# Kernel tuning notes

Hardware: AMD Instinct MI355X
Metric: run time of the kernel (lower is better)

The kernel has to match this reference:

```python
import jax, jax.numpy as jnp
import numpy as np

N_ENT = 200000; N_REL = 500; D = 400; RAP = 16; RAD = 32; H = 4; ARITY = 4; B = 512; EPS = 1e-5


def _lin(x, w, b):
    return x @ w.T + b


def _ln(x, g, b):
    m = x.mean(-1, keepdims=True)
    v = x.var(-1, keepdims=True)
    return (x - m) / jnp.sqrt(v + EPS) * g + b


def _forward(ent_emb, rel_emb, pos_emb, relposw_w, relposw_b, relposinv_w, relposinv_b,
             relw4_w, relw4_b, q_w, q_b, k_w, k_b, v_w, v_b, fca_w, fca_b,
             ln1_g, ln1_b, ln2_g, ln2_b, w1_w, w1_b, w2_w, w2_b, fc_w, fc_b,
             posbn_g, posbn_b, bn_g, bn_b, bias, rel_idx, ent_idx):
    r0 = rel_emb[rel_idx]                                   # [B,D]
    e0 = ent_emb[ent_idx]                                   # [B,A-1,D]
    x0 = jnp.concatenate([r0[:, None, :], e0], axis=1) + pos_emb[:ARITY][None]
    # manual multi-head attention (separate q/k/v/fc linears)
    q = _lin(x0, q_w, q_b).reshape(B, ARITY, H, D)
    k = _lin(x0, k_w, k_b).reshape(B, ARITY, H, D)
    v = _lin(x0, v_w, v_b).reshape(B, ARITY, H, D)
    scale = jnp.float32(1.0 / np.sqrt(D))
    att = jax.nn.softmax(jnp.einsum('blhd,bmhd->bhlm', q, k) * scale, axis=-1)
    o = jnp.einsum('bhlm,bmhd->blhd', att, v).reshape(B, ARITY, H * D)
    x1 = _ln(x0 + _lin(o, fca_w, fca_b), ln1_g, ln1_b)
    # Conv1d kernel-size-1 FFN == pointwise linear
    ffn = _lin(jax.nn.relu(_lin(x1, w1_w, w1_b)), w2_w, w2_b)
    x2 = _ln(x1 + ffn, ln2_g, ln2_b)
    r = x2[:, 0, :]
    # RA_Position: relation-generated per-sample 1x1 grouped conv filters
    f = _lin(r, relposw_w, relposw_b)                       # [B,RAP]

    def ra_pos(e):
        # BatchNorm1d(num_features=1): batch stats over (batch, length)
        m = e.mean(); vv = e.var()
        xn = (e - m) / jnp.sqrt(vv + EPS) * posbn_g[0] + posbn_b[0]
        y = (f[:, :, None] * xn[:, None, :]).reshape(B, RAP * D)  # grouped conv1d k=1
        return _lin(y, relposinv_w, relposinv_b)            # [B,D]

    ef = jnp.stack([ra_pos(x2[:, i + 1, :]) for i in range(ARITY - 1)], axis=1)  # [B,3,D]
    # RADConv: torch .view(B,1,-1,arity-1) interleaves entities -> plain row-major reshape
    xr = ef.reshape(B, 1, D, ARITY - 1)
    m = xr.mean(); vv = xr.var()                            # BatchNorm2d(1), batch stats
    xn = (xr - m) / jnp.sqrt(vv + EPS) * bn_g[0] + bn_b[0]
    kern = _lin(r, relw4_w, relw4_b).reshape(B, RAD, ARITY - 1)
    conv = jnp.einsum('bkj,bij->bki', kern, xn[:, 0])       # grouped conv2d (1,A-1), valid
    pooled = conv.reshape(B, RAD, D // 2, 2).max(axis=-1).reshape(B, RAD * D // 2)
    h = jax.nn.relu(_lin(pooled, fc_w, fc_b))               # [B,D]
    return h @ ent_emb.T + bias                             # [B,N_ENT]


def setup_inputs() -> dict:
    key = jax.random.key(0)
    ks = iter(jax.random.split(key, 40))

    def nrm(shape, s=0.05):
        return jax.random.normal(next(ks), shape, jnp.float32) * s

    def lw(o, i):
        return jax.random.normal(next(ks), (o, i), jnp.float32) * (1.0 / np.sqrt(i)).astype(np.float32)

    return {
        'ent_emb': nrm((N_ENT, D)),
        'rel_emb': nrm((N_REL, D)),
        'pos_emb': nrm((9, D)),
        'relposw_w': lw(RAP, D), 'relposw_b': jnp.zeros((RAP,), jnp.float32),
        'relposinv_w': lw(D, RAP * D), 'relposinv_b': jnp.zeros((D,), jnp.float32),
        'relw4_w': lw(3 * RAD, D), 'relw4_b': jnp.zeros((3 * RAD,), jnp.float32),
        'q_w': lw(H * D, D), 'q_b': jnp.zeros((H * D,), jnp.float32),
        'k_w': lw(H * D, D), 'k_b': jnp.zeros((H * D,), jnp.float32),
        'v_w': lw(H * D, D), 'v_b': jnp.zeros((H * D,), jnp.float32),
        'fca_w': lw(D, H * D), 'fca_b': jnp.zeros((D,), jnp.float32),
        'ln1_g': jnp.ones((D,), jnp.float32), 'ln1_b': jnp.zeros((D,), jnp.float32),
        'ln2_g': jnp.ones((D,), jnp.float32), 'ln2_b': jnp.zeros((D,), jnp.float32),
        'w1_w': lw(2 * D, D), 'w1_b': jnp.zeros((2 * D,), jnp.float32),
        'w2_w': lw(D, 2 * D), 'w2_b': jnp.zeros((D,), jnp.float32),
        'fc_w': lw(D, RAD * D // 2), 'fc_b': jnp.zeros((D,), jnp.float32),
        'posbn_g': jnp.ones((1,), jnp.float32), 'posbn_b': jnp.zeros((1,), jnp.float32),
        'bn_g': jnp.ones((1,), jnp.float32), 'bn_b': jnp.zeros((1,), jnp.float32),
        'bias': jnp.zeros((N_ENT,), jnp.float32),
        'rel_idx': jax.random.randint(next(ks), (B,), 0, N_REL),
        'ent_idx': jax.random.randint(next(ks), (B, ARITY - 1), 0, N_ENT),
    }


def reference(ent_emb, rel_emb, pos_emb, relposw_w, relposw_b, relposinv_w, relposinv_b,
              relw4_w, relw4_b, q_w, q_b, k_w, k_b, v_w, v_b, fca_w, fca_b,
              ln1_g, ln1_b, ln2_g, ln2_b, w1_w, w1_b, w2_w, w2_b, fc_w, fc_b,
              posbn_g, posbn_b, bn_g, bn_b, bias, rel_idx, ent_idx):
    return _forward(ent_emb, rel_emb, pos_emb, relposw_w, relposw_b, relposinv_w, relposinv_b,
                    relw4_w, relw4_b, q_w, q_b, k_w, k_b, v_w, v_b, fca_w, fca_b,
                    ln1_g, ln1_b, ln2_g, ln2_b, w1_w, w1_b, w2_w, w2_b, fc_w, fc_b,
                    posbn_g, posbn_b, bn_g, bn_b, bias, rel_idx, ent_idx)
```

## Files before the change

### kernel.cpp

```cpp
#include <hip/hip_runtime.h>

typedef unsigned short u16;
typedef __attribute__((ext_vector_type(8))) short s8v;
typedef __attribute__((ext_vector_type(4))) float f4v;
typedef __attribute__((ext_vector_type(4))) unsigned int u32x4;

typedef const __attribute__((address_space(1))) unsigned gas_u32;
typedef __attribute__((address_space(3))) unsigned las_u32;

__device__ __forceinline__ float bf2f(u16 u) { return __uint_as_float(((unsigned)u) << 16); }
__device__ __forceinline__ u16 f2bf(float x) {
  unsigned b = __float_as_uint(x);
  return (u16)((b + 0x7FFFu + ((b >> 16) & 1u)) >> 16);
}

__global__ void convert_w_kernel(const float* __restrict__ src, u16* __restrict__ dst,
                                 int N, int Kreal, int KP) {
  int idx = blockIdx.x * 256 + threadIdx.x;
  if (idx >= N * KP) return;
  int n = idx / KP, k = idx % KP;
  dst[idx] = (k < Kreal) ? f2bf(src[(size_t)n * Kreal + k]) : (u16)0;
}

__global__ void build_x0_kernel(const float* __restrict__ ent_emb, const float* __restrict__ rel_emb,
                                const float* __restrict__ pos_emb, const int* __restrict__ rel_idx,
                                const int* __restrict__ ent_idx, u16* __restrict__ x0) {
  int idx = blockIdx.x * 256 + threadIdx.x;
  if (idx >= 512 * 4 * 400) return;
  int d = idx % 400;
  int l = (idx / 400) % 4;
  int b = idx / 1600;
  float v;
  if (l == 0) v = rel_emb[(size_t)rel_idx[b] * 400 + d];
  else        v = ent_emb[(size_t)ent_idx[b * 3 + l - 1] * 400 + d];
  x0[(size_t)(b * 4 + l) * 416 + d] = f2bf(v + pos_emb[l * 400 + d]);
}

template<bool BF32, bool RELU, bool OUTBF>
__global__ __launch_bounds__(256) void mfma_gemm(
    const u16* __restrict__ A, int lda,
    const void* __restrict__ Bp, int ldb,
    const float* __restrict__ bias,
    void* __restrict__ Cp, long long ldc,
    int N, int KP, int Kreal) {
  __shared__ u16 As[128 * 32];
  __shared__ u16 Bs[128 * 32];
  const int m0 = blockIdx.x * 128, n0 = blockIdx.y * 128;
  const int tid = threadIdx.x;
  const int lane = tid & 63, w = tid >> 6;
  const int mw = (w & 1) * 64, nw = (w >> 1) * 64;
  f4v acc[4][4] = {};

  const int arow = tid >> 2, akq = tid & 3;
  const u16* ag0 = A + (size_t)(m0 + arow) * lda + akq * 8;
  const u16* ag1 = A + (size_t)(m0 + 64 + arow) * lda + akq * 8;
  int br0 = n0 + arow;      if (br0 >= N) br0 = N - 1;
  int br1 = n0 + 64 + arow; if (br1 >= N) br1 = N - 1;
  const u16* bg0 = nullptr; const u16* bg1 = nullptr;
  if (!BF32) {
    bg0 = (const u16*)Bp + (size_t)br0 * ldb + akq * 8;
    bg1 = (const u16*)Bp + (size_t)br1 * ldb + akq * 8;
  }
  const float* Bf = (const float*)Bp;

  u16* lA0 = As + w * 512;
  u16* lA1 = As + 2048 + w * 512;
  u16* lB0 = Bs + w * 512;
  u16* lB1 = Bs + 2048 + w * 512;

  const u16* ap = As + (size_t)(mw + (lane & 15)) * 32 + (lane >> 4) * 8;
  const u16* bp = Bs + (size_t)(nw + (lane & 15)) * 32 + (lane >> 4) * 8;

  for (int k0 = 0; k0 < KP; k0 += 32) {
    __builtin_amdgcn_global_load_lds((gas_u32*)(ag0 + k0), (las_u32*)lA0, 16, 0, 0);
    __builtin_amdgcn_global_load_lds((gas_u32*)(ag1 + k0), (las_u32*)lA1, 16, 0, 0);
    if (BF32) {
      int kk = k0 + akq * 8;
#pragma unroll
      for (int t = 0; t < 2; ++t) {
        int rowg = t ? br1 : br0;
        const float* src = Bf + (size_t)rowg * ldb + kk;
        float4 v0 = (kk < Kreal)     ? *(const float4*)(src)     : make_float4(0.f, 0.f, 0.f, 0.f);
        float4 v1 = (kk + 4 < Kreal) ? *(const float4*)(src + 4) : make_float4(0.f, 0.f, 0.f, 0.f);
        u32x4 pk;
        pk.x = (unsigned)f2bf(v0.x) | ((unsigned)f2bf(v0.y) << 16);
        pk.y = (unsigned)f2bf(v0.z) | ((unsigned)f2bf(v0.w) << 16);
        pk.z = (unsigned)f2bf(v1.x) | ((unsigned)f2bf(v1.y) << 16);
        pk.w = (unsigned)f2bf(v1.z) | ((unsigned)f2bf(v1.w) << 16);
        *(u32x4*)(Bs + t * 2048 + tid * 8) = pk;
      }
    } else {
      __builtin_amdgcn_global_load_lds((gas_u32*)(bg0 + k0), (las_u32*)lB0, 16, 0, 0);
      __builtin_amdgcn_global_load_lds((gas_u32*)(bg1 + k0), (las_u32*)lB1, 16, 0, 0);
    }
    __syncthreads();
    s8v af[4], bf[4];
#pragma unroll
    for (int i = 0; i < 4; ++i) af[i] = *(const s8v*)(ap + i * 16 * 32);
#pragma unroll
    for (int j = 0; j < 4; ++j) bf[j] = *(const s8v*)(bp + j * 16 * 32);
#pragma unroll
    for (int i = 0; i < 4; ++i)
#pragma unroll
      for (int j = 0; j < 4; ++j)
        acc[i][j] = __builtin_amdgcn_mfma_f32_16x16x32_bf16(af[i], bf[j], acc[i][j], 0, 0, 0);
    __syncthreads();
  }

  const int quad = lane >> 4, col = lane & 15;
#pragma unroll
  for (int i = 0; i < 4; ++i) {
#pragma unroll
    for (int j = 0; j < 4; ++j) {
      int n = n0 + nw + 16 * j + col;
      if (n >= N) continue;
      float bv = bias[n];
#pragma unroll
      for (int r = 0; r < 4; ++r) {
        int m = m0 + mw + 16 * i + quad * 4 + r;
        float v = acc[i][j][r] + bv;
        if (RELU) v = fmaxf(v, 0.f);
        size_t off = (size_t)m * ldc + n;
        if (OUTBF) ((u16*)Cp)[off] = f2bf(v);
        else       ((float*)Cp)[off] = v;
      }
    }
  }
}

__global__ __launch_bounds__(256) void sgemm_valu(
    const u16* __restrict__ X, int lda,
    const float* __restrict__ W, const float* __restrict__ bvec,
    float* __restrict__ Y, int ldc, int M, int N, int K) {
  int n0 = blockIdx.x * 64, m0 = blockIdx.y * 64;
  __shared__ float Xs[16][64];
  __shared__ float Ws[16][64];
  int tid = threadIdx.x;
  int tx = tid & 15, ty = tid >> 4;
  int lr = tid >> 2, lc = (tid & 3) << 2;
  float acc[4][4] = {};
  const u16* xbase = X + (size_t)(m0 + lr) * lda + lc;
  int wn = n0 + lr;
  bool wvalid = wn < N;
  const float* wbase = W + (size_t)(wvalid ? wn : 0) * K + lc;
  for (int k0 = 0; k0 < K; k0 += 16) {
#pragma unroll
    for (int j = 0; j < 4; ++j) Xs[lc + j][lr] = bf2f(xbase[k0 + j]);
#pragma unroll
    for (int j = 0; j < 4; ++j) Ws[lc + j][lr] = wvalid ? wbase[k0 + j] : 0.f;
    __syncthreads();
#pragma unroll
    for (int kk = 0; kk < 16; ++kk) {
      float xv[4], wv[4];
#pragma unroll
      for (int a = 0; a < 4; ++a) xv[a] = Xs[kk][ty * 4 + a];
#pragma unroll
      for (int b = 0; b < 4; ++b) wv[b] = Ws[kk][tx * 4 + b];
#pragma unroll
      for (int a = 0; a < 4; ++a)
#pragma unroll
        for (int b = 0; b < 4; ++b)
          acc[a][b] = fmaf(xv[a], wv[b], acc[a][b]);
    }
    __syncthreads();
  }
#pragma unroll
  for (int a = 0; a < 4; ++a) {
    int m = m0 + ty * 4 + a;
#pragma unroll
    for (int b = 0; b < 4; ++b) {
      int n = n0 + tx * 4 + b;
      if (n < N) Y[(size_t)m * ldc + n] = acc[a][b] + bvec[n];
    }
  }
}

__device__ __forceinline__ float wave_sum(float v) {
#pragma unroll
  for (int o = 32; o > 0; o >>= 1) v += __shfl_xor(v, o);
  return v;
}

__global__ void score_kernel(const u16* __restrict__ qkv, float* __restrict__ att) {
  int bh = blockIdx.x;
  int h = bh & 3, b = bh >> 2;
  int lane = threadIdx.x;
  float s[4][4];
#pragma unroll
  for (int l = 0; l < 4; ++l) {
    const u16* qp = qkv + (size_t)(b * 4 + l) * 4800 + h * 400;
#pragma unroll
    for (int m = 0; m < 4; ++m) {
      const u16* kp = qkv + (size_t)(b * 4 + m) * 4800 + 1600 + h * 400;
      float p = 0.f;
      for (int d = lane; d < 400; d += 64) p += bf2f(qp[d]) * bf2f(kp[d]);
      s[l][m] = wave_sum(p) * 0.05f;
    }
  }
  if (lane < 16) {
    int l = lane >> 2, m = lane & 3;
    float mx = fmaxf(fmaxf(s[l][0], s[l][1]), fmaxf(s[l][2], s[l][3]));
    float e0 = expf(s[l][0] - mx), e1 = expf(s[l][1] - mx);
    float e2 = expf(s[l][2] - mx), e3 = expf(s[l][3] - mx);
    float inv = 1.f / (e0 + e1 + e2 + e3);
    float ev = (m == 0) ? e0 : (m == 1) ? e1 : (m == 2) ? e2 : e3;
    att[(size_t)bh * 16 + l * 4 + m] = ev * inv;
  }
}

__global__ void attn_apply_kernel(const float* __restrict__ att, const u16* __restrict__ qkv,
                                  u16* __restrict__ o) {
  int idx = blockIdx.x * 256 + threadIdx.x;
  if (idx >= 2048 * 1600) return;
  int col = idx % 1600;
  int row = idx / 1600;
  int b = row >> 2, l = row & 3, h = col / 400;
  const float* ap = att + ((size_t)b * 4 + h) * 16 + l * 4;
  float acc = 0.f;
#pragma unroll
  for (int m = 0; m < 4; ++m)
    acc += ap[m] * bf2f(qkv[(size_t)(b * 4 + m) * 4800 + 3200 + col]);
  o[idx] = f2bf(acc);
}

__global__ __launch_bounds__(128) void ln_kernel(const u16* __restrict__ A, int lda,
                                                 const float* __restrict__ Bv, int ldb,
                                                 const float* __restrict__ g, const float* __restrict__ beta,
                                                 u16* __restrict__ out, int ldo) {
  int row = blockIdx.x;
  int tid = threadIdx.x;
  const u16* a = A + (size_t)row * lda;
  const float* bb = Bv + (size_t)row * ldb;
  float vals[4] = {};
  float s = 0.f, q = 0.f;
#pragma unroll
  for (int j = 0; j < 4; ++j) {
    int d = tid + j * 128;
    if (d < 400) { float x = bf2f(a[d]) + bb[d]; vals[j] = x; s += x; q += x * x; }
  }
  __shared__ float rs[128], rq[128];
  rs[tid] = s; rq[tid] = q;
  __syncthreads();
  for (int off = 64; off > 0; off >>= 1) {
    if (tid < off) { rs[tid] += rs[tid + off]; rq[tid] += rq[tid + off]; }
    __syncthreads();
  }
  float mean = rs[0] * (1.f / 400.f);
  float var = rq[0] * (1.f / 400.f) - mean * mean;
  float rstd = rsqrtf(var + 1e-5f);
  u16* op = out + (size_t)row * ldo;
#pragma unroll
  for (int j = 0; j < 4; ++j) {
    int d = tid + j * 128;
    if (d < 400) op[d] = f2bf((vals[j] - mean) * rstd * g[d] + beta[d]);
  }
}

template<typename T>
__global__ __launch_bounds__(256) void stat_partial(const T* __restrict__ base, long long slice_stride,
                                                    int row_stride, int len, long long total, int nb,
                                                    float* __restrict__ sums) {
  int slice = blockIdx.x / nb, chunk = blockIdx.x % nb;
  const T* p = base + (size_t)slice * slice_stride;
  int tid = threadIdx.x;
  float s = 0.f, q = 0.f;
  long long step = (long long)nb * 256;
  for (long long t = (long long)chunk * 256 + tid; t < total; t += step) {
    int row = (int)(t / len), colx = (int)(t % len);
    float x;
    if (sizeof(T) == 2) x = bf2f(((const u16*)p)[(size_t)row * row_stride + colx]);
    else                x = ((const float*)p)[(size_t)row * row_stride + colx];
    s += x; q += x * x;
  }
  __shared__ float rs[256], rq[256];
  rs[tid] = s; rq[tid] = q;
  __syncthreads();
  for (int off = 128; off > 0; off >>= 1) {
    if (tid < off) { rs[tid] += rs[tid + off]; rq[tid] += rq[tid + off]; }
    __syncthreads();
  }
  if (tid == 0) {
    atomicAdd(&sums[2 * slice], rs[0]);
    atomicAdd(&sums[2 * slice + 1], rq[0]);
  }
}

__device__ __forceinline__ void mean_rstd(const float* sums, float count, float& m, float& rstd) {
  m = sums[0] / count;
  float var = sums[1] / count - m * m;
  rstd = rsqrtf(var + 1e-5f);
}

__global__ void build_y3_kernel(const u16* __restrict__ x2, const float* __restrict__ f,
                                const float* __restrict__ scal, const float* __restrict__ pg,
                                const float* __restrict__ pb, u16* __restrict__ y3) {
  int idx = blockIdx.x * 256 + threadIdx.x;
  if (idx >= 3 * 512 * 6400) return;
  int d = idx % 400;
  int p = (idx / 400) % 16;
  int b = (idx / 6400) % 512;
  int i = idx / (512 * 6400);
  float m, rstd;
  mean_rstd(scal + 2 * i, 204800.f, m, rstd);
  float e = bf2f(x2[(size_t)(b * 4 + i + 1) * 400 + d]);
  float xn = (e - m) * rstd * pg[0] + pb[0];
  y3[idx] = f2bf(f[b * 16 + p] * xn);
}

__global__ void convpool_kernel(const float* __restrict__ kern, const float* __restrict__ efI,
                                const float* __restrict__ scal, const float* __restrict__ bg_,
                                const float* __restrict__ bb_, u16* __restrict__ pooled) {
  int idx = blockIdx.x * 256 + threadIdx.x;
  if (idx >= 512 * 32 * 200) return;
  int i2 = idx % 200;
  int k = (idx / 200) % 32;
  int b = idx / 6400;
  float m, rstd;
  mean_rstd(scal, 614400.f, m, rstd);
  float bg = bg_[0], bb = bb_[0];
  const float* kp = kern + (size_t)b * 96 + k * 3;
  float c0 = 0.f, c1 = 0.f;
#pragma unroll
  for (int j = 0; j < 3; ++j) {
    int p0 = 6 * i2 + j;
    int p1 = 6 * i2 + 3 + j;
    float e0 = efI[(size_t)(p0 / 400) * 204800 + (size_t)b * 400 + (p0 % 400)];
    float e1 = efI[(size_t)(p1 / 400) * 204800 + (size_t)b * 400 + (p1 % 400)];
    c0 += kp[j] * ((e0 - m) * rstd * bg + bb);
    c1 += kp[j] * ((e1 - m) * rstd * bg + bb);
  }
  pooled[(size_t)b * 6400 + k * 200 + i2] = f2bf(fmaxf(c0, c1));
}

extern "C" void kernel_launch(void* const* d_in, const int* in_sizes, int n_in,
                              void* d_out, int out_size, void* d_ws, size_t ws_size,
                              hipStream_t stream) {
  const float* ent_emb    = (const float*)d_in[0];
  const float* rel_emb    = (const float*)d_in[1];
  const float* pos_emb    = (const float*)d_in[2];
  const float* relposw_w  = (const float*)d_in[3];
  const float* relposw_b  = (const float*)d_in[4];
  const float* relposinv_w= (const float*)d_in[5];
  const float* relposinv_b= (const float*)d_in[6];
  const float* relw4_w    = (const float*)d_in[7];
  const float* relw4_b    = (const float*)d_in[8];
  const float* q_w        = (const float*)d_in[9];
  const float* q_b        = (const float*)d_in[10];
  const float* k_w        = (const float*)d_in[11];
  const float* k_b        = (const float*)d_in[12];
  const float* v_w        = (const float*)d_in[13];
  const float* v_b        = (const float*)d_in[14];
  const float* fca_w      = (const float*)d_in[15];
  const float* fca_b      = (const float*)d_in[16];
  const float* ln1_g      = (const float*)d_in[17];
  const float* ln1_b      = (const float*)d_in[18];
  const float* ln2_g      = (const float*)d_in[19];
  const float* ln2_b      = (const float*)d_in[20];
  const float* w1_w       = (const float*)d_in[21];
  const float* w1_b       = (const float*)d_in[22];
  const float* w2_w       = (const float*)d_in[23];
  const float* w2_b       = (const float*)d_in[24];
  const float* fc_w       = (const float*)d_in[25];
  const float* fc_b       = (const float*)d_in[26];
  const float* posbn_g    = (const float*)d_in[27];
  const float* posbn_b    = (const float*)d_in[28];
  const float* bn_g       = (const float*)d_in[29];
  const float* bn_b       = (const float*)d_in[30];
  const float* bias       = (const float*)d_in[31];
  const int*  rel_idx     = (const int*)d_in[32];
  const int*  ent_idx     = (const int*)d_in[33];

  char* base = (char*)d_ws;
  u16*   wqkv  = (u16*)(base + 0);
  u16*   wfca  = (u16*)(base + 3993600);
  u16*   ww1   = (u16*)(base + 5273600);
  u16*   ww2   = (u16*)(base + 5939200);
  u16*   wrpi  = (u16*)(base + 6579200);
  u16*   wfc   = (u16*)(base + 11699200);
  float* qkvb  = (float*)(base + 16819200);
  u16*   x0    = (u16*)(base + 16838400);
  u16*   x1    = (u16*)(base + 18542336);
  u16*   hbuf  = (u16*)(base + 20246272);
  float* att   = (float*)(base + 20672256);
  float* tmp32 = (float*)(base + 20803328);
  u16*   x2    = (u16*)(base + 24080128);
  float* fbuf  = (float*)(base + 25718528);
  float* kern  = (float*)(base + 25751296);
  float* efI   = (float*)(base + 25947904);
  float* scal  = (float*)(base + 28405504);
  u16*   qkvbuf= (u16*)(base + 28405760);
  u16*   y3    = qkvbuf;
  u16*   obuf  = (u16*)(base + 48066560);
  u16*   pooled= obuf;
  u16*   ffn1  = (u16*)(base + 54620160);

  dim3 blk(256);

  hipMemsetAsync(base + 16838400, 0, 3833856, stream);
  hipMemsetAsync(scal, 0, 64, stream);

  hipMemcpyAsync(qkvb,        q_b, 1600 * 4, hipMemcpyDeviceToDevice, stream);
  hipMemcpyAsync(qkvb + 1600, k_b, 1600 * 4, hipMemcpyDeviceToDevice, stream);
  hipMemcpyAsync(qkvb + 3200, v_b, 1600 * 4, hipMemcpyDeviceToDevice, stream);

  convert_w_kernel<<<(1600 * 416 + 255) / 256, blk, 0, stream>>>(q_w, wqkv,              1600, 400, 416);
  convert_w_kernel<<<(1600 * 416 + 255) / 256, blk, 0, stream>>>(k_w, wqkv + 1600 * 416, 1600, 400, 416);
  convert_w_kernel<<<(1600 * 416 + 255) / 256, blk, 0, stream>>>(v_w, wqkv + 3200 * 416, 1600, 400, 416);
  convert_w_kernel<<<(400 * 1600 + 255) / 256, blk, 0, stream>>>(fca_w, wfca, 400, 1600, 1600);
  convert_w_kernel<<<(800 * 416 + 255) / 256,  blk, 0, stream>>>(w1_w, ww1, 800, 400, 416);
  convert_w_kernel<<<(400 * 800 + 255) / 256,  blk, 0, stream>>>(w2_w, ww2, 400, 800, 800);
  convert_w_kernel<<<(400 * 6400 + 255) / 256, blk, 0, stream>>>(relposinv_w, wrpi, 400, 6400, 6400);
  convert_w_kernel<<<(400 * 6400 + 255) / 256, blk, 0, stream>>>(fc_w, wfc, 400, 6400, 6400);

  build_x0_kernel<<<3200, blk, 0, stream>>>(ent_emb, rel_emb, pos_emb, rel_idx, ent_idx, x0);

  mfma_gemm<false, false, true><<<dim3(16, 38), blk, 0, stream>>>(
      x0, 416, wqkv, 416, qkvb, qkvbuf, 4800, 4800, 416, 416);

  score_kernel<<<2048, 64, 0, stream>>>(qkvbuf, att);
  attn_apply_kernel<<<12800, blk, 0, stream>>>(att, qkvbuf, obuf);

  mfma_gemm<false, false, false><<<dim3(16, 4), blk, 0, stream>>>(
      obuf, 1600, wfca, 1600, fca_b, tmp32, 400, 400, 1600, 1600);
  ln_kernel<<<2048, 128, 0, stream>>>(x0, 416, tmp32, 400, ln1_g, ln1_b, x1, 416);

  mfma_gemm<false, true, true><<<dim3(16, 7), blk, 0, stream>>>(
      x1, 416, ww1, 416, w1_b, ffn1, 800, 800, 416, 416);
  mfma_gemm<false, false, false><<<dim3(16, 4), blk, 0, stream>>>(
      ffn1, 800, ww2, 800, w2_b, tmp32, 400, 400, 800, 800);
  ln_kernel<<<2048, 128, 0, stream>>>(x1, 416, tmp32, 400, ln2_g, ln2_b, x2, 400);

  sgemm_valu<<<dim3(1, 8), blk, 0, stream>>>(x2, 1600, relposw_w, relposw_b, fbuf, 16, 512, 16, 400);
  sgemm_valu<<<dim3(2, 8), blk, 0, stream>>>(x2, 1600, relw4_w, relw4_b, kern, 96, 512, 96, 400);

  stat_partial<u16><<<3 * 16, blk, 0, stream>>>(x2 + 400, 400, 1600, 400, 204800, 16, scal);

  build_y3_kernel<<<38400, blk, 0, stream>>>(x2, fbuf, scal, posbn_g, posbn_b, y3);
  mfma_gemm<false, false, false><<<dim3(12, 4), blk, 0, stream>>>(
      y3, 6400, wrpi, 6400, relposinv_b, efI, 400, 400, 6400, 6400);

  stat_partial<float><<<32, blk, 0, stream>>>(efI, 0, 400, 400, 614400, 32, scal + 6);

  convpool_kernel<<<12800, blk, 0, stream>>>(kern, efI, scal + 6, bn_g, bn_b, pooled);

  mfma_gemm<false, true, true><<<dim3(4, 4), blk, 0, stream>>>(
      pooled, 6400, wfc, 6400, fc_b, hbuf, 416, 400, 6400, 6400);

  mfma_gemm<true, false, false><<<dim3(4, 1563), blk, 0, stream>>>(
      hbuf, 416, ent_emb, 400, bias, d_out, 200000, 200000, 416, 400);
}
```

Before: 1.523 ms.

## Pre-convert entity table to bf16 and swizzle final GEMM blocks across XCDs

Adds a kernel that converts the 200000x400 fp32 entity embedding table into a padded bf16 copy in workspace, so the final scoring GEMM reads bf16 B tiles and skips the in-loop fp32 conversion. It also adds an XCD-aware block remapping for that GEMM so neighbouring tiles that share the A operand land on the same chiplet, improving L2 reuse. The conversion is an extra full pass over the 320MB table each call, and it runs only when the workspace is large enough, otherwise the fp32 path is kept but still swizzled.

```diff
diff --git a/kernel.cpp b/kernel.cpp
--- a/kernel.cpp
+++ b/kernel.cpp
@@ -20,6 +20,24 @@
   if (idx >= N * KP) return;
   int n = idx / KP, k = idx % KP;
   dst[idx] = (k < Kreal) ? f2bf(src[(size_t)n * Kreal + k]) : (u16)0;
+}
+
+__global__ __launch_bounds__(256) void convert_ent_kernel(const float* __restrict__ src,
+                                                          u16* __restrict__ dst) {
+  int idx = blockIdx.x * 256 + threadIdx.x;
+  if (idx >= 200000 * 52) return;
+  int c = idx % 52, n = idx / 52;
+  u32x4 pk = {0u, 0u, 0u, 0u};
+  if (c < 50) {
+    const float* p = src + (size_t)n * 400 + c * 8;
+    float4 v0 = *(const float4*)(p);
+    float4 v1 = *(const float4*)(p + 4);
+    pk.x = (unsigned)f2bf(v0.x) | ((unsigned)f2bf(v0.y) << 16);
+    pk.y = (unsigned)f2bf(v0.z) | ((unsigned)f2bf(v0.w) << 16);
+    pk.z = (unsigned)f2bf(v1.x) | ((unsigned)f2bf(v1.y) << 16);
+    pk.w = (unsigned)f2bf(v1.z) | ((unsigned)f2bf(v1.w) << 16);
+  }
+  *(u32x4*)(dst + (size_t)n * 416 + c * 8) = pk;
 }
 
 __global__ void build_x0_kernel(const float* __restrict__ ent_emb, const float* __restrict__ rel_emb,
@@ -36,7 +54,7 @@
   x0[(size_t)(b * 4 + l) * 416 + d] = f2bf(v + pos_emb[l * 400 + d]);
 }
 
-template<bool BF32, bool RELU, bool OUTBF>
+template<bool BF32, bool RELU, bool OUTBF, bool SWZ>
 __global__ __launch_bounds__(256) void mfma_gemm(
     const u16* __restrict__ A, int lda,
     const void* __restrict__ Bp, int ldb,
@@ -45,7 +63,20 @@
     int N, int KP, int Kreal) {
   __shared__ u16 As[128 * 32];
   __shared__ u16 Bs[128 * 32];
-  const int m0 = blockIdx.x * 128, n0 = blockIdx.y * 128;
+  int m0, n0;
+  if (SWZ) {
+    int f = blockIdx.y * gridDim.x + blockIdx.x;
+    int nwg = gridDim.x * gridDim.y;
+    int xcd = f & 7, j = f >> 3;
+    int q = nwg >> 3, r = nwg & 7;
+    int wg = (xcd < r ? xcd * (q + 1) : r * (q + 1) + (xcd - r) * q) + j;
+    int gx = gridDim.x;
+    m0 = (wg % gx) * 128;
+    n0 = (wg / gx) * 128;
+  } else {
+    m0 = blockIdx.x * 128;
+    n0 = blockIdx.y * 128;
+  }
   const int tid = threadIdx.x;
   const int lane = tid & 63, w = tid >> 6;
   const int mw = (w & 1) * 64, nw = (w >> 1) * 64;
@@ -393,6 +424,8 @@
   u16*   obuf  = (u16*)(base + 48066560);
   u16*   pooled= obuf;
   u16*   ffn1  = (u16*)(base + 54620160);
+  u16*   entbf = (u16*)(base + 57896960);
+  const bool big_ws = ws_size >= 224296960ull;
 
   dim3 blk(256);
 
@@ -414,19 +447,19 @@
 
   build_x0_kernel<<<3200, blk, 0, stream>>>(ent_emb, rel_emb, pos_emb, rel_idx, ent_idx, x0);
 
-  mfma_gemm<false, false, true><<<dim3(16, 38), blk, 0, stream>>>(
+  mfma_gemm<false, false, true, false><<<dim3(16, 38), blk, 0, stream>>>(
       x0, 416, wqkv, 416, qkvb, qkvbuf, 4800, 4800, 416, 416);
 
   score_kernel<<<2048, 64, 0, stream>>>(qkvbuf, att);
   attn_apply_kernel<<<12800, blk, 0, stream>>>(att, qkvbuf, obuf);
 
-  mfma_gemm<false, false, false><<<dim3(16, 4), blk, 0, stream>>>(
+  mfma_gemm<false, false, false, false><<<dim3(16, 4), blk, 0, stream>>>(
       obuf, 1600, wfca, 1600, fca_b, tmp32, 400, 400, 1600, 1600);
   ln_kernel<<<2048, 128, 0, stream>>>(x0, 416, tmp32, 400, ln1_g, ln1_b, x1, 416);
 
-  mfma_gemm<false, true, true><<<dim3(16, 7), blk, 0, stream>>>(
+  mfma_gemm<false, true, true, false><<<dim3(16, 7), blk, 0, stream>>>(
       x1, 416, ww1, 416, w1_b, ffn1, 800, 800, 416, 416);
-  mfma_gemm<false, false, false><<<dim3(16, 4), blk, 0, stream>>>(
+  mfma_gemm<false, false, false, false><<<dim3(16, 4), blk, 0, stream>>>(
       ffn1, 800, ww2, 800, w2_b, tmp32, 400, 400, 800, 800);
   ln_kernel<<<2048, 128, 0, stream>>>(x1, 416, tmp32, 400, ln2_g, ln2_b, x2, 400);
 
@@ -436,16 +469,22 @@
   stat_partial<u16><<<3 * 16, blk, 0, stream>>>(x2 + 400, 400, 1600, 400, 204800, 16, scal);
 
   build_y3_kernel<<<38400, blk, 0, stream>>>(x2, fbuf, scal, posbn_g, posbn_b, y3);
-  mfma_gemm<false, false, false><<<dim3(12, 4), blk, 0, stream>>>(
+  mfma_gemm<false, false, false, false><<<dim3(12, 4), blk, 0, stream>>>(
       y3, 6400, wrpi, 6400, relposinv_b, efI, 400, 400, 6400, 6400);
 
   stat_partial<float><<<32, blk, 0, stream>>>(efI, 0, 400, 400, 614400, 32, scal + 6);
 
   convpool_kernel<<<12800, blk, 0, stream>>>(kern, efI, scal + 6, bn_g, bn_b, pooled);
 
-  mfma_gemm<false, true, true><<<dim3(4, 4), blk, 0, stream>>>(
+  mfma_gemm<false, true, true, false><<<dim3(4, 4), blk, 0, stream>>>(
       pooled, 6400, wfc, 6400, fc_b, hbuf, 416, 400, 6400, 6400);
 
-  mfma_gemm<true, false, false><<<dim3(4, 1563), blk, 0, stream>>>(
-      hbuf, 416, ent_emb, 400, bias, d_out, 200000, 200000, 416, 400);
-}
+  if (big_ws) {
+    convert_ent_kernel<<<40625, blk, 0, stream>>>(ent_emb, entbf);
+    mfma_gemm<false, false, false, true><<<dim3(4, 1563), blk, 0, stream>>>(
+        hbuf, 416, entbf, 416, bias, d_out, 200000, 200000, 416, 416);
+  } else {
+    mfma_gemm<true, false, false, true><<<dim3(4, 1563), blk, 0, stream>>>(
+        hbuf, 416, ent_emb, 400, bias, d_out, 200000, 200000, 416, 400);
+  }
+}
```

After: 1.510 ms. No clear change (-0.9%).
